# Performance work log

Hardware: AMD Instinct MI355X
Metric: run time of the kernel (lower is better)

The kernel has to match this reference:

```python
import jax, jax.numpy as jnp
import numpy as np

GRID_SIZE = 5
SPLINE_ORDER = 3
NUM_BASIS = GRID_SIZE + SPLINE_ORDER  # 8
BN_EPS = 1e-5


def make_grid():
    # efficient_kan extended uniform grid on [-1, 1]
    h = 2.0 / GRID_SIZE
    return (jnp.arange(-SPLINE_ORDER, GRID_SIZE + SPLINE_ORDER + 1, dtype=jnp.float32) * h) - 1.0


def b_splines(x, grid):
    """Cox-de Boor B-spline bases. x: (...,) -> (..., NUM_BASIS)."""
    x = x[..., None]
    bases = ((x >= grid[:-1]) & (x < grid[1:])).astype(x.dtype)
    for p in range(1, SPLINE_ORDER + 1):
        left = (x - grid[: -(p + 1)]) / (grid[p:-1] - grid[: -(p + 1)])
        right = (grid[p + 1:] - x) / (grid[p + 1:] - grid[1:-p])
        bases = left * bases[..., :-1] + right * bases[..., 1:]
    return bases


def grouped_conv(x, w, groups, padding):
    return jax.lax.conv_general_dilated(
        x, w, window_strides=(1, 1), padding=[(padding, padding)] * 2,
        feature_group_count=groups,
        dimension_numbers=("NCHW", "OIHW", "NCHW"))


def kan_conv(x, w_base, b_base, w_spline, grid, groups, padding):
    # base branch: grouped conv on SiLU(x)
    base = grouped_conv(jax.nn.silu(x), w_base, groups, padding)
    base = base + b_base[None, :, None, None]
    # spline branch: per-channel B-spline basis expansion (C -> C*NUM_BASIS)
    B, C, H, W = x.shape
    sp = b_splines(jnp.moveaxis(x, 1, -1), grid)            # (B,H,W,C,NB)
    sp = jnp.moveaxis(sp.reshape(B, H, W, C * NUM_BASIS), -1, 1)  # (B,C*NB,H,W)
    return base + grouped_conv(sp, w_spline, groups, padding)


def setup_inputs() -> dict:
    key = jax.random.key(0)
    ks = jax.random.split(key, 8)
    B, C_in, C_out, G, H, W = 16, 128, 256, 8, 64, 64
    x = jax.random.normal(ks[0], (B, C_in, H, W), dtype=jnp.float32)
    w_base1 = jax.random.normal(ks[1], (C_out, C_in // G, 1, 1), jnp.float32) * 0.1
    b_base1 = jnp.zeros((C_out,), jnp.float32)
    w_spline1 = jax.random.normal(ks[2], (C_out, (C_in * NUM_BASIS) // G, 1, 1), jnp.float32) * 0.05
    w_base2 = jax.random.normal(ks[3], (C_out, C_out // G, 3, 3), jnp.float32) * 0.05
    b_base2 = jnp.zeros((C_out,), jnp.float32)
    w_spline2 = jax.random.normal(ks[4], (C_out, (C_out * NUM_BASIS) // G, 3, 3), jnp.float32) * 0.02
    gamma = jnp.ones((C_out,), jnp.float32)
    beta = jnp.zeros((C_out,), jnp.float32)
    return {"x": x, "w_base1": w_base1, "b_base1": b_base1, "w_spline1": w_spline1,
            "w_base2": w_base2, "b_base2": b_base2, "w_spline2": w_spline2,
            "gamma": gamma, "beta": beta}


def reference(x, w_base1, b_base1, w_spline1, w_base2, b_base2, w_spline2, gamma, beta):
    G = 8
    grid = make_grid()
    h = kan_conv(x, w_base1, b_base1, w_spline1, grid, G, padding=0)   # 1x1 grouped KAN conv
    h = kan_conv(h, w_base2, b_base2, w_spline2, grid, G, padding=1)   # 3x3 grouped KAN conv
    # BatchNorm2d (training mode: batch statistics over N,H,W)
    mean = jnp.mean(h, axis=(0, 2, 3), keepdims=True)
    var = jnp.var(h, axis=(0, 2, 3), keepdims=True)
    hn = (h - mean) * jax.lax.rsqrt(var + BN_EPS)
    return hn * gamma[None, :, None, None] + beta[None, :, None, None]
```

## Files before the change

kernel.cpp:

```cpp
#include <hip/hip_runtime.h>
#include <hip/hip_bf16.h>
#include <stdint.h>


#define NB 8
#define NF 9
#define CIN 128
#define COUT 256
#define GROUPS 8
#define HW 4096
#define BATCH 16

#define WFS_ELEMS 589824
#define WFB_ELEMS 73728
#define WF1S_ELEMS 32768
#define WF1B_ELEMS 8192

typedef __attribute__((ext_vector_type(8))) short bf16x8;
typedef __attribute__((ext_vector_type(4))) float f32x4;

__device__ __forceinline__ unsigned bf16r(float f) {
    union { float f; unsigned u; } c; c.f = f;
    unsigned r = c.u + 0x7FFF + ((c.u >> 16) & 1);
    return r >> 16;
}

__device__ __forceinline__ void spline_w(float v, float& w0, float& w1,
                                         float& w2, float& w3, int& k) {
    float s = (v + 2.2f) * 2.5f;
    float fk = floorf(s);
    k = (int)fk;
    float u = s - fk;
    float um = 1.0f - u;
    float u2 = u * u, u3 = u2 * u;
    w0 = um * um * um * (1.0f / 6.0f);
    w1 = (3.0f * u3 - 6.0f * u2 + 4.0f) * (1.0f / 6.0f);
    w2 = (-3.0f * u3 + 3.0f * u2 + 3.0f * u + 1.0f) * (1.0f / 6.0f);
    w3 = u3 * (1.0f / 6.0f);
}

__device__ __forceinline__ uint4 spline_row(float v, bool in, float& sv) {
    sv = v / (1.0f + __expf(-v));
    float w0, w1, w2, w3; int k;
    spline_w(v, w0, w1, w2, w3, k);
    unsigned W0, W1;
    asm("v_cvt_pk_bf16_f32 %0, %1, %2" : "=v"(W0) : "v"(w0), "v"(w1));
    asm("v_cvt_pk_bf16_f32 %0, %1, %2" : "=v"(W1) : "v"(w2), "v"(w3));
    int kk = in ? (k - 3) : 99;
    unsigned odd = (unsigned)kk & 1u;
    unsigned A = W0 << 16;
    unsigned B = (W0 >> 16) | (W1 << 16);
    unsigned C = W1 >> 16;
    unsigned t0 = odd ? A : W0;
    unsigned t1 = odd ? B : W1;
    unsigned t2 = odd ? C : 0u;
    int q = kk >> 1;
    uint4 pk;
    pk.x = (q == 0) ? t0 : (q == -1) ? t1 : (q == -2) ? t2 : 0u;
    pk.y = (q == 1) ? t0 : (q == 0)  ? t1 : (q == -1) ? t2 : 0u;
    pk.z = (q == 2) ? t0 : (q == 1)  ? t1 : (q == 0)  ? t2 : 0u;
    pk.w = (q == 3) ? t0 : (q == 2)  ? t1 : (q == 1)  ? t2 : 0u;
    return pk;
}

__global__ void __launch_bounds__(256) repack2_kernel(
    const float* __restrict__ wb1, const float* __restrict__ ws1,
    const float* __restrict__ wb2, const float* __restrict__ ws2,
    unsigned short* __restrict__ wfs, unsigned short* __restrict__ wfb,
    unsigned short* __restrict__ wf1s, unsigned short* __restrict__ wf1b) {
    int i = blockIdx.x * 256 + threadIdx.x;
    if (i < WF1S_ELEMS) {
        int j = i & 7;
        int lane = (i >> 3) & 63;
        int nf = (i >> 9) & 1;
        int cc = (i >> 10) & 3;
        int g = i >> 12;
        int c_loc = cc * 4 + (lane >> 4);
        int cog = g * 32 + nf * 16 + (lane & 15);
        wf1s[i] = (unsigned short)bf16r(ws1[cog * 128 + c_loc * 8 + j]);
    }
    if (i < WF1B_ELEMS) {
        int j = i & 7;
        int lane = (i >> 3) & 63;
        int nf = (i >> 9) & 1;
        int g = (i >> 10) & 7;
        int k = (lane >> 4) * 8 + j;
        int cog = g * 32 + nf * 16 + (lane & 15);
        wf1b[i] = (k < 16) ? (unsigned short)bf16r(wb1[cog * 16 + k]) : 0;
    }
    if (i < WFB_ELEMS) {
        int j = i & 7;
        int lane = (i >> 3) & 63;
        int nf = (i >> 9) & 1;
        int t = i >> 10;
        int dy = t % 3; t /= 3;
        int dx = t % 3; t /= 3;
        int g = t;
        int ch = (lane >> 4) * 8 + j;
        int cog = g * 32 + nf * 16 + (lane & 15);
        wfb[i] = (unsigned short)bf16r(wb2[((cog * 32 + ch) * 3 + dy) * 3 + dx]);
    }
    if (i < WFS_ELEMS) {
        int j = i & 7;
        int t = i >> 3;
        int lane = t & 63; t >>= 6;
        int nf = t & 1; t >>= 1;
        int dy = t % 3; t /= 3;
        int dx = t % 3; t /= 3;
        int cc = t & 7; t >>= 3;
        int g = t;
        int c_loc = cc * 4 + (lane >> 4);
        int cog = g * 32 + nf * 16 + (lane & 15);
        float v = ws2[((cog * 256 + c_loc * 8 + j) * 3 + dy) * 3 + dx];
        wfs[i] = (unsigned short)bf16r(v);
    }
}

__global__ void __launch_bounds__(256, 4) kan1m_kernel(
    const float* __restrict__ x, const bf16x8* __restrict__ wf1s,
    const bf16x8* __restrict__ wf1b, const float* __restrict__ bb1,
    float* __restrict__ h1) {
    __shared__ __align__(16) unsigned char lds[32768];
    unsigned char* spl = lds;
    unsigned char* slu = lds + 16384;

    const int tid = threadIdx.x;
    const int lane = tid & 63;
    const int w = tid >> 6;
    const int blk = blockIdx.x;
    const int tile = blk & 15;
    const int g = (blk >> 4) & 7;
    const int b = blk >> 7;
    const int lrow = lane & 15;
    const int lhi = lane >> 4;
    const int posg0 = tile * 256;

    {
        int key = (tid >> 1) & 3;
        uint4 z = {0, 0, 0, 0};
        *reinterpret_cast<uint4*>(slu + tid * 64 + ((2 ^ key) << 4)) = z;
        *reinterpret_cast<uint4*>(slu + tid * 64 + ((3 ^ key) << 4)) = z;
    }

    const float* xg = x + ((size_t)b * CIN + g * 16) * HW + posg0;

    float xreg[4];
#pragma unroll
    for (int it = 0; it < 4; ++it) xreg[it] = xg[it * HW + tid];

    f32x4 acc[4][2];
#pragma unroll
    for (int m = 0; m < 4; ++m)
#pragma unroll
        for (int nf = 0; nf < 2; ++nf) {
            float bias = bb1[g * 32 + nf * 16 + lrow];
            acc[m][nf] = (f32x4){bias, bias, bias, bias};
        }

    for (int cc = 0; cc < 4; ++cc) {
        __syncthreads();
        int key = (tid >> 1) & 3;
#pragma unroll
        for (int it = 0; it < 4; ++it) {
            float sv;
            uint4 pk = spline_row(xreg[it], true, sv);
            *reinterpret_cast<uint4*>(spl + tid * 64 + ((it ^ key) << 4)) = pk;
            int cg = cc * 4 + it;
            *reinterpret_cast<unsigned short*>(
                slu + tid * 64 + (((cg >> 3) ^ key) << 4) + (cg & 7) * 2) =
                (unsigned short)bf16r(sv);
        }
        if (cc < 3) {
#pragma unroll
            for (int it = 0; it < 4; ++it)
                xreg[it] = xg[((cc + 1) * 4 + it) * HW + tid];
        }
        __syncthreads();
        const bf16x8* wpc = wf1s + (size_t)((g * 4 + cc) * 2) * 64;
        bf16x8 bf0 = wpc[lane];
        bf16x8 bf1 = wpc[64 + lane];
#pragma unroll
        for (int m = 0; m < 4; ++m) {
            int pos = w * 64 + m * 16 + lrow;
            int ra = pos * 64 + ((lhi ^ ((pos >> 1) & 3)) << 4);
            bf16x8 af = *reinterpret_cast<const bf16x8*>(spl + ra);
            acc[m][0] = __builtin_amdgcn_mfma_f32_16x16x32_bf16(af, bf0, acc[m][0], 0, 0, 0);
            acc[m][1] = __builtin_amdgcn_mfma_f32_16x16x32_bf16(af, bf1, acc[m][1], 0, 0, 0);
        }
    }
    {
        const bf16x8* wpb = wf1b + (size_t)(g * 2) * 64;
        bf16x8 bf0 = wpb[lane];
        bf16x8 bf1 = wpb[64 + lane];
#pragma unroll
        for (int m = 0; m < 4; ++m) {
            int pos = w * 64 + m * 16 + lrow;
            int ra = pos * 64 + ((lhi ^ ((pos >> 1) & 3)) << 4);
            bf16x8 af = *reinterpret_cast<const bf16x8*>(slu + ra);
            acc[m][0] = __builtin_amdgcn_mfma_f32_16x16x32_bf16(af, bf0, acc[m][0], 0, 0, 0);
            acc[m][1] = __builtin_amdgcn_mfma_f32_16x16x32_bf16(af, bf1, acc[m][1], 0, 0, 0);
        }
    }
#pragma unroll
    for (int m = 0; m < 4; ++m)
#pragma unroll
        for (int nf = 0; nf < 2; ++nf) {
            int co = g * 32 + nf * 16 + lrow;
            float4 o = {acc[m][nf][0], acc[m][nf][1], acc[m][nf][2], acc[m][nf][3]};
            *reinterpret_cast<float4*>(
                &h1[((size_t)b * COUT + co) * HW + posg0 + w * 64 + m * 16 + lhi * 4]) = o;
        }
}

__device__ __forceinline__ void stage_elem(
    unsigned char* __restrict__ spl, unsigned char* __restrict__ slu,
    float v, bool in, int waddrS, int p, int cg) {
    float sv;
    uint4 pk = spline_row(v, in, sv);
    *reinterpret_cast<uint4*>(spl + waddrS) = pk;
    int key = (p >> 1) & 3;
    *reinterpret_cast<unsigned short*>(
        slu + p * 64 + (((cg >> 3) ^ key) << 4) + ((cg * 2) & 15)) =
        (unsigned short)bf16r(sv);
}

__device__ __forceinline__ void mfma_hr(
    const unsigned char* __restrict__ spl, const bf16x8 (&bf)[3][2],
    int pbase, int lhi, f32x4 (&acc)[4][2]) {
#pragma unroll
    for (int hr = 0; hr < 6; ++hr) {
        int p = pbase + hr * 18;
        int ra = p * 64 + ((lhi ^ ((p >> 1) & 3)) << 4);
        bf16x8 af = *reinterpret_cast<const bf16x8*>(spl + ra);
#pragma unroll
        for (int dy = 0; dy < 3; ++dy) {
            int y = hr - dy;
            if (y >= 0 && y < 4) {
                acc[y][0] = __builtin_amdgcn_mfma_f32_16x16x32_bf16(af, bf[dy][0], acc[y][0], 0, 0, 0);
                acc[y][1] = __builtin_amdgcn_mfma_f32_16x16x32_bf16(af, bf[dy][1], acc[y][1], 0, 0, 0);
            }
        }
    }
}

__global__ void __launch_bounds__(256, 3) kan2_mfma3_kernel(
    const float* __restrict__ h1, const bf16x8* __restrict__ wfs,
    const bf16x8* __restrict__ wfb, const float* __restrict__ bb2,
    float* __restrict__ h2, float* __restrict__ partial2) {
    __shared__ __align__(16) unsigned char lds[41472];
    unsigned char* spl = lds;
    unsigned char* slu = lds + 20736;

    const int tid = threadIdx.x;
    const int lane = tid & 63;
    const int w = tid >> 6;
    const int blk = blockIdx.x;
    const int tile = blk & 15;
    const int g = (blk >> 4) & 7;
    const int b = blk >> 7;
    const int ty = (tile >> 2) * 16, tx = (tile & 3) * 16;
    const int lrow = lane & 15;
    const int lhi = lane >> 4;

    int chv[6], pv[6], offv[6], wadS[6];
#pragma unroll
    for (int it = 0; it < 6; ++it) {
        int e = tid + it * 256;
        int ch = (e * 3237) >> 20;
        int p = e - ch * 324;
        int hy = (p * 57) >> 10;
        int hx = p - hy * 18;
        int iy = ty + hy - 1, ix = tx + hx - 1;
        bool in = ((unsigned)iy < 64u) & ((unsigned)ix < 64u);
        chv[it] = ch;
        pv[it] = p;
        offv[it] = in ? (iy * 64 + ix) : -1;
        int key = (p >> 1) & 3;
        wadS[it] = p * 64 + ((ch ^ key) << 4);
    }

    const float* h1g = h1 + (size_t)(b * COUT + g * 32) * HW;

    float vreg[6];
#pragma unroll
    for (int it = 0; it < 6; ++it) {
        if (it < 5 || tid < 16)
            vreg[it] = (offv[it] >= 0) ? h1g[chv[it] * HW + offv[it]] : 0.0f;
    }

    f32x4 acc[4][2];
#pragma unroll
    for (int y = 0; y < 4; ++y)
#pragma unroll
        for (int nf = 0; nf < 2; ++nf) {
            float bias = bb2[g * 32 + nf * 16 + lrow];
            acc[y][nf] = (f32x4){bias, bias, bias, bias};
        }

    const int pbase0 = (w * 4) * 18 + lrow;

    for (int cc = 0; cc < 8; ++cc) {
        const bf16x8* wpc = wfs + (size_t)((g * 8 + cc) * 18) * 64;
        bf16x8 bfA[3][2];
#pragma unroll
        for (int dy = 0; dy < 3; ++dy)
#pragma unroll
            for (int nf = 0; nf < 2; ++nf)
                bfA[dy][nf] = wpc[(dy * 2 + nf) * 64 + lane];

        __syncthreads();
#pragma unroll
        for (int it = 0; it < 6; ++it) {
            if (it < 5 || tid < 16)
                stage_elem(spl, slu, vreg[it], offv[it] >= 0, wadS[it],
                           pv[it], cc * 4 + chv[it]);
        }
        if (cc < 7) {
#pragma unroll
            for (int it = 0; it < 6; ++it) {
                if (it < 5 || tid < 16)
                    vreg[it] = (offv[it] >= 0)
                        ? h1g[((cc + 1) * 4 + chv[it]) * HW + offv[it]] : 0.0f;
            }
        }
        __syncthreads();

#pragma unroll
        for (int dx = 0; dx < 3; ++dx) {
            bf16x8 bfB[3][2];
            if (dx < 2) {
                const bf16x8* wpn = wpc + (size_t)((dx + 1) * 6) * 64;
#pragma unroll
                for (int dy = 0; dy < 3; ++dy)
#pragma unroll
                    for (int nf = 0; nf < 2; ++nf)
                        bfB[dy][nf] = wpn[(dy * 2 + nf) * 64 + lane];
            }
            mfma_hr(spl, bfA, pbase0 + dx, lhi, acc);
            if (dx < 2) {
#pragma unroll
                for (int dy = 0; dy < 3; ++dy)
#pragma unroll
                    for (int nf = 0; nf < 2; ++nf)
                        bfA[dy][nf] = bfB[dy][nf];
            }
        }
    }

#pragma unroll
    for (int dx = 0; dx < 3; ++dx) {
        bf16x8 bf[3][2];
        const bf16x8* wp = wfb + (size_t)(((g * 3 + dx) * 3) * 2) * 64;
#pragma unroll
        for (int dy = 0; dy < 3; ++dy)
#pragma unroll
            for (int nf = 0; nf < 2; ++nf)
                bf[dy][nf] = wp[(dy * 2 + nf) * 64 + lane];
        mfma_hr(slu, bf, pbase0 + dx, lhi, acc);
    }

#pragma unroll
    for (int y = 0; y < 4; ++y) {
        int oy = ty + w * 4 + y;
#pragma unroll
        for (int nf = 0; nf < 2; ++nf) {
            int co = g * 32 + nf * 16 + lrow;
            float4 o = {acc[y][nf][0], acc[y][nf][1], acc[y][nf][2], acc[y][nf][3]};
            *reinterpret_cast<float4*>(
                &h2[(((size_t)b * COUT + co) * 64 + oy) * 64 + tx + lhi * 4]) = o;
        }
    }

    float s0 = 0.0f, q0 = 0.0f, s1 = 0.0f, q1 = 0.0f;
#pragma unroll
    for (int y = 0; y < 4; ++y)
#pragma unroll
        for (int i = 0; i < 4; ++i) {
            float a0 = acc[y][0][i], a1 = acc[y][1][i];
            s0 += a0; q0 = fmaf(a0, a0, q0);
            s1 += a1; q1 = fmaf(a1, a1, q1);
        }
    s0 += __shfl_xor(s0, 16); s0 += __shfl_xor(s0, 32);
    q0 += __shfl_xor(q0, 16); q0 += __shfl_xor(q0, 32);
    s1 += __shfl_xor(s1, 16); s1 += __shfl_xor(s1, 32);
    q1 += __shfl_xor(q1, 16); q1 += __shfl_xor(q1, 32);
    __syncthreads();
    float* stb = reinterpret_cast<float*>(lds);
    if (lane < 16) {
        int base = (w * 16 + lane) * 4;
        stb[base] = s0; stb[base + 1] = q0;
        stb[base + 2] = s1; stb[base + 3] = q1;
    }
    __syncthreads();
    if (tid < 64) {
        int slot = tid >> 1;
        int j = tid & 1;
        int lr = slot & 15, nf = slot >> 4;
        float a = 0.0f;
#pragma unroll
        for (int wv = 0; wv < 4; ++wv)
            a += stb[(wv * 16 + lr) * 4 + nf * 2 + j];
        partial2[blk * 64 + tid] = a;
    }
}

__global__ void __launch_bounds__(256) bnstat2_kernel(
    const float* __restrict__ partial2, const float* __restrict__ gamma,
    const float* __restrict__ beta, float* __restrict__ stats) {
    int co = blockIdx.x;
    int t = threadIdx.x;
    int g = co >> 5, loc = co & 31;
    int b = t >> 4, tile = t & 15;
    int blk = (b * 8 + g) * 16 + tile;
    float s = partial2[blk * 64 + loc * 2];
    float ss = partial2[blk * 64 + loc * 2 + 1];
    __shared__ float r1[256], r2[256];
    r1[t] = s; r2[t] = ss;
    __syncthreads();
    for (int o = 128; o > 0; o >>= 1) {
        if (t < o) { r1[t] += r1[t + o]; r2[t] += r2[t + o]; }
        __syncthreads();
    }
    if (t == 0) {
        const float invn = 1.0f / 65536.0f;
        float mean = r1[0] * invn;
        float var = r2[0] * invn - mean * mean;
        float sc = gamma[co] * rsqrtf(var + 1e-5f);
        stats[2 * co] = sc;
        stats[2 * co + 1] = beta[co] - mean * sc;
    }
}

__global__ void __launch_bounds__(256) bnapply_kernel(
    float* __restrict__ h2, const float* __restrict__ stats, int n4) {
    int i = blockIdx.x * 256 + threadIdx.x;
    if (i >= n4) return;
    int co = (i >> 10) & 255;
    float sc = stats[2 * co], sh = stats[2 * co + 1];
    float4 v = reinterpret_cast<float4*>(h2)[i];
    float4 o;
    o.x = fmaf(v.x, sc, sh);
    o.y = fmaf(v.y, sc, sh);
    o.z = fmaf(v.z, sc, sh);
    o.w = fmaf(v.w, sc, sh);
    reinterpret_cast<float4*>(h2)[i] = o;
}

extern "C" void kernel_launch(void* const* d_in, const int* in_sizes, int n_in,
                              void* d_out, int out_size, void* d_ws, size_t ws_size,
                              hipStream_t stream) {
    const float* x   = (const float*)d_in[0];
    const float* wb1 = (const float*)d_in[1];
    const float* bb1 = (const float*)d_in[2];
    const float* ws1 = (const float*)d_in[3];
    const float* wb2 = (const float*)d_in[4];
    const float* bb2 = (const float*)d_in[5];
    const float* ws2 = (const float*)d_in[6];
    const float* gamma = (const float*)d_in[7];
    const float* beta  = (const float*)d_in[8];

    char* ws = (char*)d_ws;
    unsigned short* wfs  = (unsigned short*)ws;
    unsigned short* wfb  = (unsigned short*)(ws + 1179648);
    unsigned short* wf1s = (unsigned short*)(ws + 1327104);
    unsigned short* wf1b = (unsigned short*)(ws + 1392640);
    float* partial2 = (float*)(ws + 1409024);
    float* stats    = (float*)(ws + 1933312);
    float* h1       = (float*)(ws + 1935360);

    float* h2 = (float*)d_out;

    repack2_kernel<<<(WFS_ELEMS + 255) / 256, 256, 0, stream>>>(
        wb1, ws1, wb2, ws2, wfs, wfb, wf1s, wf1b);
    kan1m_kernel<<<BATCH * GROUPS * 16, 256, 0, stream>>>(
        x, (const bf16x8*)wf1s, (const bf16x8*)wf1b, bb1, h1);
    kan2_mfma3_kernel<<<BATCH * GROUPS * 16, 256, 0, stream>>>(
        h1, (const bf16x8*)wfs, (const bf16x8*)wfb, bb2, h2, partial2);
    bnstat2_kernel<<<COUT, 256, 0, stream>>>(partial2, gamma, beta, stats);
    bnapply_kernel<<<(4194304 + 255) / 256, 256, 0, stream>>>(
        h2, stats, 4194304);
}
```

Before: 157.5 us.

## Software-pipeline spline expansion and loads two chunks ahead of MFMA work in kan2

Restructures the conv2 channel-chunk loop so the B-spline expansion of the next chunk runs between the MFMA phases of the current chunk, and global loads of h1 are issued two chunks ahead. The LDS stores now write precomputed packed values, and the channel offset is folded into the gather offset. MFMA sections are wrapped in s_setprio to favour the matrix work among waves. This adds register pressure from the held expanded values (uint4 x6 plus scalars), which could cause spills or lower occupancy under the 3-blocks launch bound.

```diff
diff --git a/kernel.cpp b/kernel.cpp
--- a/kernel.cpp
+++ b/kernel.cpp
@@ -63,6 +63,13 @@
     return pk;
 }
 
+__device__ __forceinline__ void expand_elem(float v, bool in,
+                                            uint4& pk, unsigned& su) {
+    float sv;
+    pk = spline_row(v, in, sv);
+    su = bf16r(sv);
+}
+
 __global__ void __launch_bounds__(256) repack2_kernel(
     const float* __restrict__ wb1, const float* __restrict__ ws1,
     const float* __restrict__ wb2, const float* __restrict__ ws2,
@@ -212,16 +219,17 @@
         }
 }
 
-__device__ __forceinline__ void stage_elem(
+__device__ __forceinline__ void stage_write(
     unsigned char* __restrict__ spl, unsigned char* __restrict__ slu,
-    float v, bool in, int waddrS, int p, int cg) {
-    float sv;
-    uint4 pk = spline_row(v, in, sv);
-    *reinterpret_cast<uint4*>(spl + waddrS) = pk;
+    const uint4& pk, unsigned su, int wadS, int cc) {
+    *reinterpret_cast<uint4*>(spl + wadS) = pk;
+    int p = wadS >> 6;
     int key = (p >> 1) & 3;
+    int ch = ((wadS >> 4) & 3) ^ key;
+    int cg = cc * 4 + ch;
     *reinterpret_cast<unsigned short*>(
         slu + p * 64 + (((cg >> 3) ^ key) << 4) + ((cg * 2) & 15)) =
-        (unsigned short)bf16r(sv);
+        (unsigned short)su;
 }
 
 __device__ __forceinline__ void mfma_hr(
@@ -243,7 +251,7 @@
     }
 }
 
-__global__ void __launch_bounds__(256, 3) kan2_mfma3_kernel(
+__global__ void __launch_bounds__(256, 3) kan2_mfma4_kernel(
     const float* __restrict__ h1, const bf16x8* __restrict__ wfs,
     const bf16x8* __restrict__ wfb, const float* __restrict__ bb2,
     float* __restrict__ h2, float* __restrict__ partial2) {
@@ -262,7 +270,7 @@
     const int lrow = lane & 15;
     const int lhi = lane >> 4;
 
-    int chv[6], pv[6], offv[6], wadS[6];
+    int offv[6], wadS[6];
 #pragma unroll
     for (int it = 0; it < 6; ++it) {
         int e = tid + it * 256;
@@ -272,9 +280,7 @@
         int hx = p - hy * 18;
         int iy = ty + hy - 1, ix = tx + hx - 1;
         bool in = ((unsigned)iy < 64u) & ((unsigned)ix < 64u);
-        chv[it] = ch;
-        pv[it] = p;
-        offv[it] = in ? (iy * 64 + ix) : -1;
+        offv[it] = in ? (ch * HW + iy * 64 + ix) : -1;
         int key = (p >> 1) & 3;
         wadS[it] = p * 64 + ((ch ^ key) << 4);
     }
@@ -282,11 +288,20 @@
     const float* h1g = h1 + (size_t)(b * COUT + g * 32) * HW;
 
     float vreg[6];
-#pragma unroll
-    for (int it = 0; it < 6; ++it) {
+    uint4 ereg[6];
+    unsigned sreg[6];
+#pragma unroll
+    for (int it = 0; it < 6; ++it)
         if (it < 5 || tid < 16)
-            vreg[it] = (offv[it] >= 0) ? h1g[chv[it] * HW + offv[it]] : 0.0f;
-    }
+            vreg[it] = (offv[it] >= 0) ? h1g[offv[it]] : 0.0f;
+#pragma unroll
+    for (int it = 0; it < 6; ++it)
+        if (it < 5 || tid < 16)
+            expand_elem(vreg[it], offv[it] >= 0, ereg[it], sreg[it]);
+#pragma unroll
+    for (int it = 0; it < 6; ++it)
+        if (it < 5 || tid < 16)
+            vreg[it] = (offv[it] >= 0) ? h1g[4 * HW + offv[it]] : 0.0f;
 
     f32x4 acc[4][2];
 #pragma unroll
@@ -310,41 +325,51 @@
 
         __syncthreads();
 #pragma unroll
-        for (int it = 0; it < 6; ++it) {
+        for (int it = 0; it < 6; ++it)
             if (it < 5 || tid < 16)
-                stage_elem(spl, slu, vreg[it], offv[it] >= 0, wadS[it],
-                           pv[it], cc * 4 + chv[it]);
-        }
+                stage_write(spl, slu, ereg[it], sreg[it], wadS[it], cc);
+        __syncthreads();
+
+        bf16x8 bfB[3][2];
+#pragma unroll
+        for (int dy = 0; dy < 3; ++dy)
+#pragma unroll
+            for (int nf = 0; nf < 2; ++nf)
+                bfB[dy][nf] = wpc[(6 + dy * 2 + nf) * 64 + lane];
+        __builtin_amdgcn_s_setprio(1);
+        mfma_hr(spl, bfA, pbase0 + 0, lhi, acc);
+        __builtin_amdgcn_s_setprio(0);
+#pragma unroll
+        for (int dy = 0; dy < 3; ++dy)
+#pragma unroll
+            for (int nf = 0; nf < 2; ++nf) {
+                bfA[dy][nf] = bfB[dy][nf];
+                bfB[dy][nf] = wpc[(12 + dy * 2 + nf) * 64 + lane];
+            }
+        __builtin_amdgcn_s_setprio(1);
+        mfma_hr(spl, bfA, pbase0 + 1, lhi, acc);
+        __builtin_amdgcn_s_setprio(0);
         if (cc < 7) {
 #pragma unroll
-            for (int it = 0; it < 6; ++it) {
+            for (int it = 0; it < 6; ++it)
+                if (it < 5 || tid < 16)
+                    expand_elem(vreg[it], offv[it] >= 0, ereg[it], sreg[it]);
+        }
+        if (cc < 6) {
+#pragma unroll
+            for (int it = 0; it < 6; ++it)
                 if (it < 5 || tid < 16)
                     vreg[it] = (offv[it] >= 0)
-                        ? h1g[((cc + 1) * 4 + chv[it]) * HW + offv[it]] : 0.0f;
-            }
-        }
-        __syncthreads();
-
-#pragma unroll
-        for (int dx = 0; dx < 3; ++dx) {
-            bf16x8 bfB[3][2];
-            if (dx < 2) {
-                const bf16x8* wpn = wpc + (size_t)((dx + 1) * 6) * 64;
-#pragma unroll
-                for (int dy = 0; dy < 3; ++dy)
-#pragma unroll
-                    for (int nf = 0; nf < 2; ++nf)
-                        bfB[dy][nf] = wpn[(dy * 2 + nf) * 64 + lane];
-            }
-            mfma_hr(spl, bfA, pbase0 + dx, lhi, acc);
-            if (dx < 2) {
-#pragma unroll
-                for (int dy = 0; dy < 3; ++dy)
-#pragma unroll
-                    for (int nf = 0; nf < 2; ++nf)
-                        bfA[dy][nf] = bfB[dy][nf];
-            }
-        }
+                        ? h1g[(size_t)((cc + 2) * 4) * HW + offv[it]] : 0.0f;
+        }
+#pragma unroll
+        for (int dy = 0; dy < 3; ++dy)
+#pragma unroll
+            for (int nf = 0; nf < 2; ++nf)
+                bfA[dy][nf] = bfB[dy][nf];
+        __builtin_amdgcn_s_setprio(1);
+        mfma_hr(spl, bfA, pbase0 + 2, lhi, acc);
+        __builtin_amdgcn_s_setprio(0);
     }
 
 #pragma unroll
@@ -356,7 +381,9 @@
 #pragma unroll
             for (int nf = 0; nf < 2; ++nf)
                 bf[dy][nf] = wp[(dy * 2 + nf) * 64 + lane];
+        __builtin_amdgcn_s_setprio(1);
         mfma_hr(slu, bf, pbase0 + dx, lhi, acc);
+        __builtin_amdgcn_s_setprio(0);
     }
 
 #pragma unroll
@@ -474,7 +501,7 @@
         wb1, ws1, wb2, ws2, wfs, wfb, wf1s, wf1b);
     kan1m_kernel<<<BATCH * GROUPS * 16, 256, 0, stream>>>(
         x, (const bf16x8*)wf1s, (const bf16x8*)wf1b, bb1, h1);
-    kan2_mfma3_kernel<<<BATCH * GROUPS * 16, 256, 0, stream>>>(
+    kan2_mfma4_kernel<<<BATCH * GROUPS * 16, 256, 0, stream>>>(
         h1, (const bf16x8*)wfs, (const bf16x8*)wfb, bb2, h2, partial2);
     bnstat2_kernel<<<COUT, 256, 0, stream>>>(partial2, gamma, beta, stats);
     bnapply_kernel<<<(4194304 + 255) / 256, 256, 0, stream>>>(
```

After: 156.6 us. No clear change (-0.6%).
